# Kernel optimization log

Measured on AMD Instinct MI355X. Metric: run time of the kernel, lower is better.

The kernel has to match this reference:

```python
import jax, jax.numpy as jnp
import numpy as np

NEG = -1e30

def setup_inputs() -> dict:
    key = jax.random.key(0)
    k1, k2, k3, k4, k5, k6, k7, k8 = jax.random.split(key, 8)
    B, Ti, Tm = 4, 512, 1024
    Din, Dmem, D = 256, 256, 64
    inputs = jax.random.normal(k1, (B, Ti, Din), dtype=jnp.float32)
    memory = jax.random.normal(k2, (B, Tm, Dmem), dtype=jnp.float32)
    input_lengths = jax.random.randint(k3, (B,), 1, Ti + 1)
    memory_lengths = jax.random.randint(k4, (B,), 1, Tm + 1)
    s_in = 1.0 / np.sqrt(Din)
    s_d = 1.0 / np.sqrt(D)
    W_in = jax.random.uniform(k5, (D, Din), jnp.float32, -s_in, s_in)
    b_in = jax.random.uniform(k6, (D,), jnp.float32, -s_in, s_in)
    W_mem = jax.random.uniform(k7, (D, Dmem), jnp.float32, -s_in, s_in)
    W_final = jax.random.uniform(k8, (D,), jnp.float32, -s_d, s_d)
    return {"inputs": inputs, "memory": memory,
            "input_lengths": input_lengths, "memory_lengths": memory_lengths,
            "W_in": W_in, "b_in": b_in, "W_mem": W_mem, "W_final": W_final}

def reference(inputs, memory, input_lengths, memory_lengths, W_in, b_in, W_mem, W_final):
    # inputs: (B,Ti,Din), memory: (B,Tm,Dmem)
    input_item = jnp.einsum('bid,td->bit', inputs, W_in) + b_in      # (B,Ti,D)
    memory_item = jnp.einsum('bmd,td->bmt', memory, W_mem)           # (B,Tm,D)
    items = jnp.tanh(input_item[:, :, None, :] + memory_item[:, None, :, :])  # (B,Ti,Tm,D)
    score = jnp.einsum('bitd,d->bit'.replace('t', 'mt')[:0] or 'bimd,d->bim', items, W_final)  # (B,Ti,Tm)
    Ti = inputs.shape[-2]
    Tm = memory.shape[-2]
    in_mask = jnp.arange(Ti)[None, :] < input_lengths[:, None]       # (B,Ti)
    mem_mask = jnp.arange(Tm)[None, :] < memory_lengths[:, None]     # (B,Tm)
    score = jnp.where(in_mask[:, :, None], score, NEG)
    score = jnp.where(mem_mask[:, None, :], score, NEG)
    attn = jax.nn.softmax(score, axis=-1)                            # (B,Ti,Tm)
    out = jnp.einsum('bim,bmd->bid', attn, memory)                   # (B,Ti,Dmem)
    return out
```

## Files before the change

kernel.cpp:

```cpp
#include <hip/hip_runtime.h>

#define C2  2.8853900817779268f
#define L2E 1.4426950408889634f

typedef float float2v __attribute__((ext_vector_type(2)));

__device__ __forceinline__ float2v pk_fma(float2v a, float2v b, float2v c) {
  float2v d;
  asm("v_pk_fma_f32 %0, %1, %2, %3" : "=v"(d) : "v"(a), "v"(b), "v"(c));
  return d;
}
__device__ __forceinline__ float2v pk_fma_bl(float2v a, float2v b, float2v c) {
  float2v d;
  asm("v_pk_fma_f32 %0, %1, %2, %3 op_sel:[0,0,0] op_sel_hi:[1,0,1]"
      : "=v"(d) : "v"(a), "v"(b), "v"(c));
  return d;
}
__device__ __forceinline__ float2v pk_fma_bh(float2v a, float2v b, float2v c) {
  float2v d;
  asm("v_pk_fma_f32 %0, %1, %2, %3 op_sel:[0,1,0] op_sel_hi:[1,1,1]"
      : "=v"(d) : "v"(a), "v"(b), "v"(c));
  return d;
}

__global__ __launch_bounds__(256) void proj_kernel(
    const float* __restrict__ inputs, const float* __restrict__ memory,
    const float* __restrict__ W_in, const float* __restrict__ b_in,
    const float* __restrict__ W_mem,
    float* __restrict__ in_item, float* __restrict__ mem_itemT)
{
  const int NIN = 2048;
  int blk = blockIdx.x;
  int dg = blk & 3;
  int r0 = (blk >> 2) * 16;
  int tid = threadIdx.x;
  int dl = tid & 15;
  int rw = tid >> 4;
  int d  = dg * 16 + dl;

  __shared__ float4 wlds[16][64];

  bool is_in = (r0 < NIN);
  const float* Wsel  = is_in ? W_in  : W_mem;
  const float* Abase = is_in ? inputs : memory;
  int ar0 = is_in ? r0 : r0 - NIN;

  const float4* Wv = reinterpret_cast<const float4*>(Wsel + (size_t)dg * 16 * 256);
  #pragma unroll
  for (int u = 0; u < 4; ++u) {
    int e = tid + u * 256;
    int j = e >> 6, k4 = e & 63;
    wlds[j][k4 ^ (j & 7)] = Wv[e];
  }
  float bias = is_in ? b_in[d] : 0.f;
  __syncthreads();

  const float4* A0 = reinterpret_cast<const float4*>(Abase + (size_t)(ar0 + rw) * 256);
  float2v acc = {0.f, 0.f};
  #pragma unroll 8
  for (int k4 = 0; k4 < 64; ++k4) {
    float4 w = wlds[dl][k4 ^ (dl & 7)];
    float4 a = A0[k4];
    acc = pk_fma(float2v{a.x, a.y}, float2v{w.x, w.y}, acc);
    acc = pk_fma(float2v{a.z, a.w}, float2v{w.z, w.w}, acc);
  }
  float val = (acc.x + acc.y + bias) * C2;
  int row = ar0 + rw;
  if (is_in) {
    in_item[(size_t)row * 64 + d] = val;
  } else {
    int b_ = row >> 10, m = row & 1023;
    mem_itemT[((size_t)(b_ * 16 + (d >> 2)) * 1024 + m) * 4 + (d & 3)] = val;
  }
}

__global__ __launch_bounds__(256, 4) void attn_kernel(
    const float* __restrict__ in_item,
    const float* __restrict__ mem_itemT,
    const float* __restrict__ memory,
    const int* __restrict__ in_len, const int* __restrict__ mem_len,
    const float* __restrict__ W_final,
    float* __restrict__ o_part,
    float* __restrict__ psum_part,
    int m_count)
{
  const int Ti = 512, Tm = 1024, DM = 256;
  const int TI = 4, MT = 64;
  const int NT = m_count >> 6;
  int lin = blockIdx.x;
  int b, z, it;
  if (m_count == 512) { b = lin & 3; z = (lin >> 2) & 1; it = lin >> 3; }
  else                { b = lin & 3; z = 0;              it = lin >> 2; }
  int i0 = it * TI;
  int m_begin = z * m_count;
  int tid = threadIdx.x;

  __shared__ float4 mt[16 * 64];
  __shared__ float4 pt4[2][64];
  __shared__ float  qs[TI][64];
  __shared__ float  red[4];

  const int s_ii = __builtin_amdgcn_readfirstlane(tid >> 6);
  const int s_ml = tid & 63;
  const int dq = tid & 63, wv_ = tid >> 6;

  qs[tid >> 6][tid & 63] = in_item[((size_t)b * Ti + i0 + (tid >> 6)) * 64 + (tid & 63)];

  float Wsum = 0.f;
  #pragma unroll
  for (int j = 0; j < 64; ++j) Wsum += W_final[j];
  const float c1 = L2E * Wsum;
  const float4* Wf4 = reinterpret_cast<const float4*>(W_final);

  int ilen = in_len[b], mlen = mem_len[b];
  const bool row_valid = (i0 + s_ii) < ilen;

  const float4* mT4 = reinterpret_cast<const float4*>(mem_itemT);
  const int bb16 = b * 16;
  const float* memb = memory + (size_t)b * Tm * DM;

  float psum = 0.f;
  float2v a0x = {0,0}, a0z = {0,0}, a1x = {0,0}, a1z = {0,0};
  float2v a2x = {0,0}, a2z = {0,0}, a3x = {0,0}, a3z = {0,0};

  #pragma unroll
  for (int u = 0; u < 4; ++u) {
    int e = tid + u * 256;
    int d4 = e >> 6, mm = e & 63;
    mt[d4 * 64 + mm] = mT4[(size_t)(bb16 + d4) * 1024 + m_begin + mm];
  }
  __syncthreads();

  const float4* qrow4 = reinterpret_cast<const float4*>(qs[s_ii]);

  #pragma unroll 1
  for (int t = 0; t < NT; ++t) {
    int m0 = m_begin + t * MT;

    {
      float4 S4 = make_float4(0.f, 0.f, 0.f, 0.f);
      #pragma unroll
      for (int d4 = 0; d4 < 16; ++d4) {
        float4 mv = mt[d4 * 64 + s_ml];
        float4 qv = qrow4[d4];
        float4 w  = Wf4[d4];
        S4.x = fmaf(w.x, __builtin_amdgcn_rcpf(1.0f + __builtin_amdgcn_exp2f(qv.x + mv.x)), S4.x);
        S4.y = fmaf(w.y, __builtin_amdgcn_rcpf(1.0f + __builtin_amdgcn_exp2f(qv.y + mv.y)), S4.y);
        S4.z = fmaf(w.z, __builtin_amdgcn_rcpf(1.0f + __builtin_amdgcn_exp2f(qv.z + mv.z)), S4.z);
        S4.w = fmaf(w.w, __builtin_amdgcn_rcpf(1.0f + __builtin_amdgcn_exp2f(qv.w + mv.w)), S4.w);
      }
      float S = (S4.x + S4.y) + (S4.z + S4.w);
      int mi = m0 + s_ml;
      float p = row_valid ? ((mi < mlen) ? __builtin_amdgcn_exp2f(fmaf(-C2, S, c1)) : 0.f)
                          : 1.0f;
      reinterpret_cast<float*>(&pt4[t & 1][s_ml])[s_ii] = p;
      psum += p;
    }
    __syncthreads();

    if (t + 1 < NT) {
      int mb = m_begin + (t + 1) * MT;
      #pragma unroll
      for (int u = 0; u < 4; ++u) {
        int e = tid + u * 256;
        int d4 = e >> 6, mm = e & 63;
        mt[d4 * 64 + mm] = mT4[(size_t)(bb16 + d4) * 1024 + mb + mm];
      }
    }

    {
      const float* mpb = memb + (size_t)(m0 + wv_ * 16) * DM + dq * 4;
      #pragma unroll
      for (int mm = 0; mm < 16; ++mm) {
        float4 v  = *reinterpret_cast<const float4*>(mpb + (size_t)mm * DM);
        float4 pp = pt4[t & 1][wv_ * 16 + mm];
        float2v vx = {v.x, v.y}, vz = {v.z, v.w};
        float2v pxy = {pp.x, pp.y}, pzw = {pp.z, pp.w};
        a0x = pk_fma_bl(vx, pxy, a0x);  a0z = pk_fma_bl(vz, pxy, a0z);
        a1x = pk_fma_bh(vx, pxy, a1x);  a1z = pk_fma_bh(vz, pxy, a1z);
        a2x = pk_fma_bl(vx, pzw, a2x);  a2z = pk_fma_bl(vz, pzw, a2z);
        a3x = pk_fma_bh(vx, pzw, a3x);  a3z = pk_fma_bh(vz, pzw, a3z);
      }
    }
    __syncthreads();
  }

  {
    float s = psum;
    #pragma unroll
    for (int o = 32; o >= 1; o >>= 1) s += __shfl_xor(s, o);
    if (dq == 0) red[wv_] = s;
  }
  float4* osl = &mt[0];
  osl[(wv_ * 4 + 0) * 64 + dq] = make_float4(a0x.x, a0x.y, a0z.x, a0z.y);
  osl[(wv_ * 4 + 1) * 64 + dq] = make_float4(a1x.x, a1x.y, a1z.x, a1z.y);
  osl[(wv_ * 4 + 2) * 64 + dq] = make_float4(a2x.x, a2x.y, a2z.x, a2z.y);
  osl[(wv_ * 4 + 3) * 64 + dq] = make_float4(a3x.x, a3x.y, a3z.x, a3z.y);
  __syncthreads();

  {
    int ii = tid >> 6, d2 = tid & 63;
    float4 s = osl[ii * 64 + d2];
    #pragma unroll
    for (int w = 1; w < 4; ++w) {
      float4 v = osl[(w * 4 + ii) * 64 + d2];
      s.x += v.x; s.y += v.y; s.z += v.z; s.w += v.w;
    }
    size_t r = (size_t)b * Ti + i0 + ii;
    reinterpret_cast<float4*>(o_part)[((size_t)z * 2048 + r) * 64 + d2] = s;
  }
  if (tid < TI) {
    psum_part[(size_t)z * 2048 + (size_t)b * Ti + i0 + tid] = red[tid];
  }
}

__global__ __launch_bounds__(256) void combine_kernel(
    const float* __restrict__ o_part, const float* __restrict__ psum_part,
    float* __restrict__ out, int nsplit)
{
  int e = blockIdx.x * 256 + threadIdx.x;
  int r = e >> 6;
  const float4* op4 = reinterpret_cast<const float4*>(o_part);
  float4 o = op4[e];
  float s = psum_part[r];
  if (nsplit == 2) {
    float4 o1 = op4[e + 131072];
    o.x += o1.x; o.y += o1.y; o.z += o1.z; o.w += o1.w;
    s += psum_part[r + 2048];
  }
  float inv = __builtin_amdgcn_rcpf(s);
  o.x *= inv; o.y *= inv; o.z *= inv; o.w *= inv;
  reinterpret_cast<float4*>(out)[e] = o;
}

extern "C" void kernel_launch(void* const* d_in, const int* in_sizes, int n_in,
                              void* d_out, int out_size, void* d_ws, size_t ws_size,
                              hipStream_t stream) {
  const float* inputs   = (const float*)d_in[0];
  const float* memory   = (const float*)d_in[1];
  const int*   in_len   = (const int*)  d_in[2];
  const int*   mem_len  = (const int*)  d_in[3];
  const float* W_in     = (const float*)d_in[4];
  const float* b_in     = (const float*)d_in[5];
  const float* W_mem    = (const float*)d_in[6];
  const float* W_final  = (const float*)d_in[7];
  float* out = (float*)d_out;

  float* in_item   = (float*)d_ws;
  float* mem_itemT = in_item + 2048 * 64;
  float* o_part    = mem_itemT + 4096 * 64;
  float* psum_part = o_part + 2 * 2048 * 256;

  size_t need2 = (size_t)(131072 + 262144 + 2 * 524288 + 2 * 2048 + 64) * 4;
  int nsplit = (ws_size >= need2) ? 2 : 1;

  proj_kernel<<<1536, 256, 0, stream>>>(inputs, memory, W_in, b_in, W_mem,
                                        in_item, mem_itemT);
  attn_kernel<<<dim3(512 * nsplit), 256, 0, stream>>>(
      in_item, mem_itemT, memory, in_len, mem_len, W_final,
      o_part, psum_part, 1024 / nsplit);
  combine_kernel<<<512, 256, 0, stream>>>(o_part, psum_part, out, nsplit);
}
```

Before: 76.13 us.

## Make attention waves independent, drop LDS staging, and allow four-way memory split

The attention kernel now gives each wave its own input row and its own whole 64-wide memory tile. Each wave reads the transposed memory projection straight from global memory instead of staging it cooperatively in shared memory, and accumulates the full 256-wide output for its row itself. This removes the per-tile block barriers and the final cross-wave shared-memory reduction, and the occupancy hint rises to 6 blocks. Launch logic can now split the memory axis four ways when workspace allows, adding more blocks and more partial sums for the combine kernel. The cost is that every wave reloads mem_itemT and memory rows on its own, with no reuse across the four rows in a block, so global and cache traffic goes up. The wave-local write to ps followed by reads from other lanes also relies on implicit wave synchronisation.

```diff
diff --git a/kernel.cpp b/kernel.cpp
--- a/kernel.cpp
+++ b/kernel.cpp
@@ -74,7 +74,7 @@
   }
 }
 
-__global__ __launch_bounds__(256, 4) void attn_kernel(
+__global__ __launch_bounds__(256, 6) void attn_kernel(
     const float* __restrict__ in_item,
     const float* __restrict__ mem_itemT,
     const float* __restrict__ memory,
@@ -82,29 +82,26 @@
     const float* __restrict__ W_final,
     float* __restrict__ o_part,
     float* __restrict__ psum_part,
-    int m_count)
+    int m_count, int shift)
 {
   const int Ti = 512, Tm = 1024, DM = 256;
-  const int TI = 4, MT = 64;
+  const int MT = 64;
   const int NT = m_count >> 6;
   int lin = blockIdx.x;
-  int b, z, it;
-  if (m_count == 512) { b = lin & 3; z = (lin >> 2) & 1; it = lin >> 3; }
-  else                { b = lin & 3; z = 0;              it = lin >> 2; }
-  int i0 = it * TI;
+  int c = lin & ((1 << shift) - 1);
+  int b = c & 3;
+  int z = c >> 2;
+  int i0 = (lin >> shift) << 2;
   int m_begin = z * m_count;
   int tid = threadIdx.x;
-
-  __shared__ float4 mt[16 * 64];
-  __shared__ float4 pt4[2][64];
-  __shared__ float  qs[TI][64];
-  __shared__ float  red[4];
-
-  const int s_ii = __builtin_amdgcn_readfirstlane(tid >> 6);
-  const int s_ml = tid & 63;
-  const int dq = tid & 63, wv_ = tid >> 6;
-
-  qs[tid >> 6][tid & 63] = in_item[((size_t)b * Ti + i0 + (tid >> 6)) * 64 + (tid & 63)];
+  int lane = tid & 63;
+  int wv = tid >> 6;
+
+  __shared__ float qs[4][64];
+  __shared__ float ps[4][64];
+
+  int row = i0 + wv;
+  qs[wv][lane] = in_item[((size_t)b * Ti + row) * 64 + lane];
 
   float Wsum = 0.f;
   #pragma unroll
@@ -113,105 +110,61 @@
   const float4* Wf4 = reinterpret_cast<const float4*>(W_final);
 
   int ilen = in_len[b], mlen = mem_len[b];
-  const bool row_valid = (i0 + s_ii) < ilen;
+  const bool row_valid = row < ilen;
 
   const float4* mT4 = reinterpret_cast<const float4*>(mem_itemT);
   const int bb16 = b * 16;
-  const float* memb = memory + (size_t)b * Tm * DM;
+  const float* memb = memory + (size_t)b * Tm * DM + (size_t)lane * 4;
 
   float psum = 0.f;
-  float2v a0x = {0,0}, a0z = {0,0}, a1x = {0,0}, a1z = {0,0};
-  float2v a2x = {0,0}, a2z = {0,0}, a3x = {0,0}, a3z = {0,0};
-
-  #pragma unroll
-  for (int u = 0; u < 4; ++u) {
-    int e = tid + u * 256;
-    int d4 = e >> 6, mm = e & 63;
-    mt[d4 * 64 + mm] = mT4[(size_t)(bb16 + d4) * 1024 + m_begin + mm];
-  }
-  __syncthreads();
-
-  const float4* qrow4 = reinterpret_cast<const float4*>(qs[s_ii]);
+  float2v ax = {0.f, 0.f}, az = {0.f, 0.f};
+
+  const float4*  qrow4 = reinterpret_cast<const float4*>(qs[wv]);
+  const float2v* ps2   = reinterpret_cast<const float2v*>(ps[wv]);
 
   #pragma unroll 1
   for (int t = 0; t < NT; ++t) {
     int m0 = m_begin + t * MT;
 
-    {
-      float4 S4 = make_float4(0.f, 0.f, 0.f, 0.f);
-      #pragma unroll
-      for (int d4 = 0; d4 < 16; ++d4) {
-        float4 mv = mt[d4 * 64 + s_ml];
-        float4 qv = qrow4[d4];
-        float4 w  = Wf4[d4];
-        S4.x = fmaf(w.x, __builtin_amdgcn_rcpf(1.0f + __builtin_amdgcn_exp2f(qv.x + mv.x)), S4.x);
-        S4.y = fmaf(w.y, __builtin_amdgcn_rcpf(1.0f + __builtin_amdgcn_exp2f(qv.y + mv.y)), S4.y);
-        S4.z = fmaf(w.z, __builtin_amdgcn_rcpf(1.0f + __builtin_amdgcn_exp2f(qv.z + mv.z)), S4.z);
-        S4.w = fmaf(w.w, __builtin_amdgcn_rcpf(1.0f + __builtin_amdgcn_exp2f(qv.w + mv.w)), S4.w);
-      }
-      float S = (S4.x + S4.y) + (S4.z + S4.w);
-      int mi = m0 + s_ml;
-      float p = row_valid ? ((mi < mlen) ? __builtin_amdgcn_exp2f(fmaf(-C2, S, c1)) : 0.f)
-                          : 1.0f;
-      reinterpret_cast<float*>(&pt4[t & 1][s_ml])[s_ii] = p;
-      psum += p;
+    float4 S4 = make_float4(0.f, 0.f, 0.f, 0.f);
+    #pragma unroll 4
+    for (int d4 = 0; d4 < 16; ++d4) {
+      float4 mv = mT4[(size_t)(bb16 + d4) * 1024 + m0 + lane];
+      float4 qv = qrow4[d4];
+      float4 w  = Wf4[d4];
+      S4.x = fmaf(w.x, __builtin_amdgcn_rcpf(1.0f + __builtin_amdgcn_exp2f(qv.x + mv.x)), S4.x);
+      S4.y = fmaf(w.y, __builtin_amdgcn_rcpf(1.0f + __builtin_amdgcn_exp2f(qv.y + mv.y)), S4.y);
+      S4.z = fmaf(w.z, __builtin_amdgcn_rcpf(1.0f + __builtin_amdgcn_exp2f(qv.z + mv.z)), S4.z);
+      S4.w = fmaf(w.w, __builtin_amdgcn_rcpf(1.0f + __builtin_amdgcn_exp2f(qv.w + mv.w)), S4.w);
     }
-    __syncthreads();
-
-    if (t + 1 < NT) {
-      int mb = m_begin + (t + 1) * MT;
-      #pragma unroll
-      for (int u = 0; u < 4; ++u) {
-        int e = tid + u * 256;
-        int d4 = e >> 6, mm = e & 63;
-        mt[d4 * 64 + mm] = mT4[(size_t)(bb16 + d4) * 1024 + mb + mm];
-      }
+    float S = (S4.x + S4.y) + (S4.z + S4.w);
+    int mi = m0 + lane;
+    float p = row_valid ? ((mi < mlen) ? __builtin_amdgcn_exp2f(fmaf(-C2, S, c1)) : 0.f)
+                        : 1.0f;
+    ps[wv][lane] = p;
+    psum += p;
+
+    const float* mpb = memb + (size_t)m0 * DM;
+    #pragma unroll 4
+    for (int mm = 0; mm < 32; ++mm) {
+      float2v pp = ps2[mm];
+      float4 v0 = *reinterpret_cast<const float4*>(mpb + (size_t)(2 * mm) * DM);
+      float4 v1 = *reinterpret_cast<const float4*>(mpb + (size_t)(2 * mm + 1) * DM);
+      ax = pk_fma_bl(float2v{v0.x, v0.y}, pp, ax);
+      az = pk_fma_bl(float2v{v0.z, v0.w}, pp, az);
+      ax = pk_fma_bh(float2v{v1.x, v1.y}, pp, ax);
+      az = pk_fma_bh(float2v{v1.z, v1.w}, pp, az);
     }
-
-    {
-      const float* mpb = memb + (size_t)(m0 + wv_ * 16) * DM + dq * 4;
-      #pragma unroll
-      for (int mm = 0; mm < 16; ++mm) {
-        float4 v  = *reinterpret_cast<const float4*>(mpb + (size_t)mm * DM);
-        float4 pp = pt4[t & 1][wv_ * 16 + mm];
-        float2v vx = {v.x, v.y}, vz = {v.z, v.w};
-        float2v pxy = {pp.x, pp.y}, pzw = {pp.z, pp.w};
-        a0x = pk_fma_bl(vx, pxy, a0x);  a0z = pk_fma_bl(vz, pxy, a0z);
-        a1x = pk_fma_bh(vx, pxy, a1x);  a1z = pk_fma_bh(vz, pxy, a1z);
-        a2x = pk_fma_bl(vx, pzw, a2x);  a2z = pk_fma_bl(vz, pzw, a2z);
-        a3x = pk_fma_bh(vx, pzw, a3x);  a3z = pk_fma_bh(vz, pzw, a3z);
-      }
-    }
-    __syncthreads();
-  }
-
-  {
-    float s = psum;
-    #pragma unroll
-    for (int o = 32; o >= 1; o >>= 1) s += __shfl_xor(s, o);
-    if (dq == 0) red[wv_] = s;
-  }
-  float4* osl = &mt[0];
-  osl[(wv_ * 4 + 0) * 64 + dq] = make_float4(a0x.x, a0x.y, a0z.x, a0z.y);
-  osl[(wv_ * 4 + 1) * 64 + dq] = make_float4(a1x.x, a1x.y, a1z.x, a1z.y);
-  osl[(wv_ * 4 + 2) * 64 + dq] = make_float4(a2x.x, a2x.y, a2z.x, a2z.y);
-  osl[(wv_ * 4 + 3) * 64 + dq] = make_float4(a3x.x, a3x.y, a3z.x, a3z.y);
-  __syncthreads();
-
-  {
-    int ii = tid >> 6, d2 = tid & 63;
-    float4 s = osl[ii * 64 + d2];
-    #pragma unroll
-    for (int w = 1; w < 4; ++w) {
-      float4 v = osl[(w * 4 + ii) * 64 + d2];
-      s.x += v.x; s.y += v.y; s.z += v.z; s.w += v.w;
-    }
-    size_t r = (size_t)b * Ti + i0 + ii;
-    reinterpret_cast<float4*>(o_part)[((size_t)z * 2048 + r) * 64 + d2] = s;
-  }
-  if (tid < TI) {
-    psum_part[(size_t)z * 2048 + (size_t)b * Ti + i0 + tid] = red[tid];
-  }
+  }
+
+  float s = psum;
+  #pragma unroll
+  for (int o = 32; o >= 1; o >>= 1) s += __shfl_xor(s, o);
+
+  size_t r = (size_t)b * Ti + row;
+  reinterpret_cast<float4*>(o_part)[((size_t)z * 2048 + r) * 64 + lane] =
+      make_float4(ax.x, ax.y, az.x, az.y);
+  if (lane == 0) psum_part[(size_t)z * 2048 + r] = s;
 }
 
 __global__ __launch_bounds__(256) void combine_kernel(
@@ -221,12 +174,12 @@
   int e = blockIdx.x * 256 + threadIdx.x;
   int r = e >> 6;
   const float4* op4 = reinterpret_cast<const float4*>(o_part);
-  float4 o = op4[e];
-  float s = psum_part[r];
-  if (nsplit == 2) {
-    float4 o1 = op4[e + 131072];
-    o.x += o1.x; o.y += o1.y; o.z += o1.z; o.w += o1.w;
-    s += psum_part[r + 2048];
+  float4 o = make_float4(0.f, 0.f, 0.f, 0.f);
+  float s = 0.f;
+  for (int zi = 0; zi < nsplit; ++zi) {
+    float4 t = op4[(size_t)zi * 131072 + e];
+    o.x += t.x; o.y += t.y; o.z += t.z; o.w += t.w;
+    s += psum_part[(size_t)zi * 2048 + r];
   }
   float inv = __builtin_amdgcn_rcpf(s);
   o.x *= inv; o.y *= inv; o.z *= inv; o.w *= inv;
@@ -249,15 +202,20 @@
   float* in_item   = (float*)d_ws;
   float* mem_itemT = in_item + 2048 * 64;
   float* o_part    = mem_itemT + 4096 * 64;
-  float* psum_part = o_part + 2 * 2048 * 256;
-
-  size_t need2 = (size_t)(131072 + 262144 + 2 * 524288 + 2 * 2048 + 64) * 4;
-  int nsplit = (ws_size >= need2) ? 2 : 1;
+
+  size_t base_f  = 131072 + 262144;
+  size_t need4 = (base_f + 4 * 524288 + 4 * 2048 + 64) * 4;
+  size_t need2 = (base_f + 2 * 524288 + 2 * 2048 + 64) * 4;
+  int nsplit, shift;
+  if      (ws_size >= need4) { nsplit = 4; shift = 4; }
+  else if (ws_size >= need2) { nsplit = 2; shift = 3; }
+  else                       { nsplit = 1; shift = 2; }
+  float* psum_part = o_part + (size_t)nsplit * 2048 * 256;
 
   proj_kernel<<<1536, 256, 0, stream>>>(inputs, memory, W_in, b_in, W_mem,
                                         in_item, mem_itemT);
   attn_kernel<<<dim3(512 * nsplit), 256, 0, stream>>>(
       in_item, mem_itemT, memory, in_len, mem_len, W_final,
-      o_part, psum_part, 1024 / nsplit);
+      o_part, psum_part, 1024 / nsplit, shift);
   combine_kernel<<<512, 256, 0, stream>>>(o_part, psum_part, out, nsplit);
 }
```

Result: slower. 100.3 us (+31.7%).
